# Kernel tuning notes

Measured on AMD Instinct MI355X. Metric: run time of the kernel, lower is better.

Reference implementation:

```python
import jax, jax.numpy as jnp
import numpy as np
from jax import lax

N = 100000   # input points
M = 100000   # output points
CIN = 64
COUT = 64
K = 3        # cubic kernel size
G = 50       # grid side (points live at voxel centers of a G^3 grid)
SHIFT = 1    # coordinate shift so border queries (coord -1) stay non-negative
B = 64       # per-axis encode base, > G + K; key fits easily in int32


def _encode(c):
    # c: [..., 3] int32 xyz voxel coords -> unique int32 key
    c = c + SHIFT
    return (c[..., 2] * B + c[..., 1]) * B + c[..., 0]


def setup_inputs() -> dict:
    rng = np.random.RandomState(0)
    total = G ** 3

    def decode(idx):
        x = idx % G
        y = (idx // G) % G
        z = idx // (G * G)
        # +0.5 moves points to voxel centers (as in the layer's docstring example)
        return np.stack([x, y, z], axis=1).astype(np.float32) + 0.5

    inp_positions = jnp.asarray(decode(rng.permutation(total)[:N]))
    out_positions = jnp.asarray(decode(rng.permutation(total)[:M]))

    key = jax.random.key(0)
    k1, k2 = jax.random.split(key, 2)
    inp_features = jax.random.normal(k1, (N, CIN), jnp.float32)
    kernel = jax.random.normal(k2, (K, K, K, CIN, COUT), jnp.float32) * 0.05
    bias = jnp.zeros((COUT,), jnp.float32)
    voxel_size = jnp.ones((), jnp.float32)
    return {
        "inp_features": inp_features,
        "inp_positions": inp_positions,
        "out_positions": out_positions,
        "voxel_size": voxel_size,
        "kernel": kernel,
        "bias": bias,
    }


def reference(inp_features, inp_positions, out_positions, voxel_size, kernel, bias):
    # SparseConv on a regular grid: odd cubic kernel -> offset = 0, Linf radius
    # K*voxel*0.51 selects exactly the K^3 voxel neighborhood. Nearest-neighbor
    # interpolation with identity mapping maps relative offset d in [-r, r]^3
    # to filter tap index d + r on each axis (x = width = last spatial dim).
    inp_coord = jnp.floor(inp_positions / voxel_size).astype(jnp.int32)  # [N,3]
    out_coord = jnp.floor(out_positions / voxel_size).astype(jnp.int32)  # [M,3]

    # sorted-key hash table over input voxels
    keys = _encode(inp_coord)                    # [N]
    order = jnp.argsort(keys)
    skeys = keys[order]
    feats = inp_features[order]                  # [N, Cin]

    r = K // 2
    K3 = K ** 3
    ks = jnp.arange(K3)
    # flat kernel order is (z, y, x) to match kernel.reshape(K3, Cin, Cout)
    d_xyz = jnp.stack([ks % K - r, (ks // K) % K - r, ks // (K * K) - r],
                      axis=1).astype(jnp.int32)  # [K3, 3]
    Kmat = kernel.reshape(K3, CIN, COUT)

    n_inp = skeys.shape[0]

    def step(acc, xs):
        d, W = xs                                 # d: [3], W: [Cin, Cout]
        qk = _encode(out_coord + d)               # [M]
        p = jnp.searchsorted(skeys, qk)
        pc = jnp.clip(p, 0, n_inp - 1)
        found = (skeys[pc] == qk)[:, None]        # [M, 1]
        g = jnp.where(found, feats[pc], 0.0)      # [M, Cin]
        return acc + g @ W, None

    out0 = jnp.zeros((out_coord.shape[0], COUT), inp_features.dtype)
    out, _ = lax.scan(step, out0, (d_xyz, Kmat))
    return out + bias
```

## Files before the change

kernel.cpp:

```cpp
#include <hip/hip_runtime.h>
#include <math.h>

#define GY 54
#define ZD 58
#define NROWS (ZD*GY*64)

#define HX 10
#define HY 6
#define HXY 60
#define NH 600
#define NBX 7
#define NBY 13
#define NBZ 7
#define NBRICK (NBX*NBY*NBZ)
#define SLAB 80

#define K3CC (27*64*64)

typedef __bf16  bf16x8 __attribute__((ext_vector_type(8)));
typedef float  f32x16 __attribute__((ext_vector_type(16)));

#define AS1 __attribute__((address_space(1)))
#define AS3 __attribute__((address_space(3)))
#define GLD_LDS16(g, l) \
    __builtin_amdgcn_global_load_lds((const AS1 void*)(g), (AS3 void*)(l), 16, 0, 0)

__global__ void prep_kernel(const float* __restrict__ ipos, int n,
                            const float* __restrict__ opos, int m,
                            const float* __restrict__ vsp,
                            const float* __restrict__ W,
                            const float* __restrict__ feats,
                            int* __restrict__ imap, int* __restrict__ ikey,
                            int* __restrict__ omap, int* __restrict__ okey,
                            __bf16* __restrict__ Wt4,
                            __bf16* __restrict__ zrow,
                            __bf16* __restrict__ featsB) {
    int i = blockIdx.x * 256 + threadIdx.x;
    float vs = vsp[0];
    if (i < n) {
        int x = (int)floorf(ipos[3*i+0] / vs) + 1;
        int y = (int)floorf(ipos[3*i+1] / vs) + 1;
        int z = (int)floorf(ipos[3*i+2] / vs) + 1;
        int key = (z * GY + y) * 64 + x;
        ikey[i] = key;
        imap[key] = i;
    } else if (i < n + m) {
        int j = i - n;
        int x = (int)floorf(opos[3*j+0] / vs) + 1;
        int y = (int)floorf(opos[3*j+1] / vs) + 1;
        int z = (int)floorf(opos[3*j+2] / vs) + 1;
        int key = (z * GY + y) * 64 + x;
        okey[j] = key;
        omap[key] = j;
    } else if (i < n + m + K3CC) {
        int k  = i - n - m;
        int t  = k >> 12;
        int r  = k & 4095;
        int ci = r >> 6;
        int co = r & 63;
        int p   = ci >> 4;
        int cil = ci & 15;
        Wt4[(((p * 27 + t) << 6) + co) * 16 + cil] = (__bf16)W[k];
    } else if (i < n + m + K3CC + 32) {
        zrow[i - n - m - K3CC] = (__bf16)0.f;
    } else {
        int j = i - n - m - K3CC - 32;
        if (j < n * 8) {
            const float4* s = (const float4*)(feats + (size_t)j * 8);
            float4 f0 = s[0], f1 = s[1];
            bf16x8 v;
            v[0]=(__bf16)f0.x; v[1]=(__bf16)f0.y; v[2]=(__bf16)f0.z; v[3]=(__bf16)f0.w;
            v[4]=(__bf16)f1.x; v[5]=(__bf16)f1.y; v[6]=(__bf16)f1.z; v[7]=(__bf16)f1.w;
            *(bf16x8*)(featsB + (size_t)j * 8) = v;
        }
    }
}

#define TAP_BODY(t)                                                            \
    {                                                                          \
        const int drow = ((t)/9 - 1)*HXY + (((t)/3)%3 - 1)*HX + ((t)%3 - 1);   \
        bf16x8 a0 = *(const bf16x8*)(Ab0 + drow * 16);                         \
        bf16x8 a1 = *(const bf16x8*)(Ab0 + (drow + HXY) * 16);                 \
        bf16x8 b0 = *(const bf16x8*)(Bg0 + (t) * 1024);                        \
        bf16x8 b1 = *(const bf16x8*)(Bg0 + (t) * 1024 + 512);                  \
        acc00 = __builtin_amdgcn_mfma_f32_32x32x16_bf16(a0, b0, acc00, 0, 0, 0); \
        acc01 = __builtin_amdgcn_mfma_f32_32x32x16_bf16(a0, b1, acc01, 0, 0, 0); \
        acc10 = __builtin_amdgcn_mfma_f32_32x32x16_bf16(a1, b0, acc10, 0, 0, 0); \
        acc11 = __builtin_amdgcn_mfma_f32_32x32x16_bf16(a1, b1, acc11, 0, 0, 0); \
    }

__global__ __launch_bounds__(256, 2) void conv_kernel(
    const __bf16* __restrict__ featsB,
    const __bf16* __restrict__ Wt4,
    const __bf16* __restrict__ zrow,
    const float* __restrict__ bias,
    const int*   __restrict__ imap,
    const int*   __restrict__ ikey,
    const int*   __restrict__ omap,
    const int*   __restrict__ okey,
    float*       __restrict__ out,
    int N, int M)
{
    __shared__ __align__(16) __bf16 halo[2 * NH * 16];
    __shared__ int ridx[NH];
    __shared__ int obuf[256];

    const int tid = threadIdx.x;

    int q = (blockIdx.x & 7) * SLAB + (blockIdx.x >> 3);
    if (q >= NBRICK) return;
    const int bx = q % NBX;
    int rem = q / NBX;
    const int by = rem % NBY;
    const int bz = rem / NBY;

    #pragma unroll
    for (int it = 0; it < 3; ++it) {
        int r = it * 256 + tid;
        if (r < NH) {
            int xs = r % HX;
            int t2 = r / HX;
            int ys = t2 % HY;
            int zs = t2 / HY;
            int key = ((bz*8 + zs) * GY + (by*4 + ys)) * 64 + (bx*8 + xs);
            int idx = imap[key];
            int c = min(max(idx, 0), N - 1);
            ridx[r] = (idx >= 0 && idx < N && ikey[c] == key) ? idx : -1;
        }
    }
    {
        int x = tid & 7, y = (tid >> 3) & 3, z = tid >> 5;
        int key = ((bz*8 + z + 1) * GY + (by*4 + y + 1)) * 64 + (bx*8 + x + 1);
        int o = omap[key];
        int c = min(max(o, 0), M - 1);
        obuf[tid] = (o >= 0 && o < M && okey[c] == key) ? o : -1;
    }

    const int wave  = tid >> 6;
    const int lane  = tid & 63;
    const int lrow  = lane & 31;
    const int halfk = lane >> 5;
    const int xv = lrow & 7, yv = (lrow >> 3) & 3;
    const int arow0 = (2*wave + 1) * HXY + (yv + 1) * HX + (xv + 1);

    f32x16 acc00, acc01, acc10, acc11;
    #pragma unroll
    for (int i = 0; i < 16; ++i) { acc00[i]=0.f; acc01[i]=0.f; acc10[i]=0.f; acc11[i]=0.f; }

    __syncthreads();

    #pragma unroll
    for (int it = 0; it < 5; ++it) {
        int task = it * 256 + tid;
        if (task < NH * 2) {
            int r  = task >> 1;
            int hl = task & 1;
            int idx = ridx[r];
            const __bf16* src = (idx >= 0) ? featsB + (size_t)idx * 64 + hl * 8
                                           : zrow;
            GLD_LDS16(src, (char*)halo + task * 16);
        }
    }
    __syncthreads();

    #pragma unroll 1
    for (int p = 0; p < 4; ++p) {
        if (p < 3) {
            char* dst = (char*)halo + ((p + 1) & 1) * (NH * 16 * 2);
            #pragma unroll
            for (int it = 0; it < 5; ++it) {
                int task = it * 256 + tid;
                if (task < NH * 2) {
                    int r  = task >> 1;
                    int hl = task & 1;
                    int idx = ridx[r];
                    const __bf16* src = (idx >= 0)
                        ? featsB + (size_t)idx * 64 + (p + 1) * 16 + hl * 8
                        : zrow;
                    GLD_LDS16(src, dst + task * 16);
                }
            }
        }

        const __bf16* Ab0 = halo + (p & 1) * (NH * 16) + arow0 * 16 + halfk * 8;
        const __bf16* Bg0 = Wt4 + (size_t)p * 27648 + lrow * 16 + halfk * 8;

        #pragma unroll
        for (int t = 0; t < 27; ++t) TAP_BODY(t)

        if (p < 3) __syncthreads();
    }

    const int col0 = lrow, col1 = 32 + lrow;
    const float bv0 = bias[col0], bv1 = bias[col1];
    #pragma unroll
    for (int r = 0; r < 16; ++r) {
        int mrow = (r & 3) + 8 * (r >> 2) + 4 * halfk;
        int o0 = obuf[(2*wave)     * 32 + mrow];
        int o1 = obuf[(2*wave + 1) * 32 + mrow];
        if (o0 >= 0) {
            out[(size_t)o0 * 64 + col0] = acc00[r] + bv0;
            out[(size_t)o0 * 64 + col1] = acc01[r] + bv1;
        }
        if (o1 >= 0) {
            out[(size_t)o1 * 64 + col0] = acc10[r] + bv0;
            out[(size_t)o1 * 64 + col1] = acc11[r] + bv1;
        }
    }
}

extern "C" void kernel_launch(void* const* d_in, const int* in_sizes, int n_in,
                              void* d_out, int out_size, void* d_ws, size_t ws_size,
                              hipStream_t stream) {
    const float* feats = (const float*)d_in[0];
    const float* ipos  = (const float*)d_in[1];
    const float* opos  = (const float*)d_in[2];
    const float* vsp   = (const float*)d_in[3];
    const float* W     = (const float*)d_in[4];
    const float* bias  = (const float*)d_in[5];

    int N = in_sizes[0] / 64;
    int M = out_size / 64;

    int*    imap   = (int*)d_ws;
    int*    omap   = imap + NROWS;
    int*    ikey   = omap + NROWS;
    int*    okey   = ikey + N;
    __bf16* Wt4    = (__bf16*)(okey + M);
    __bf16* zrow   = Wt4 + K3CC;
    __bf16* featsB = zrow + 32;

    int total = N + M + K3CC + 32 + N * 8;
    prep_kernel<<<(total + 255) / 256, 256, 0, stream>>>(ipos, N, opos, M, vsp, W, feats,
                                                         imap, ikey, omap, okey,
                                                         Wt4, zrow, featsB);
    conv_kernel<<<8 * SLAB, 256, 0, stream>>>(featsB, Wt4, zrow, bias,
                                              imap, ikey, omap, okey,
                                              (float*)d_out, N, M);
}
```

Baseline: 133.5 us.

## Split input-channel reduction across two blocks per brick with atomic accumulation

Each spatial brick is now handled by two blocks, each covering half of the input-channel chunks. Partial sums are combined with float atomicAdd into an output that the prep kernel pre-fills with bias. This doubles the grid and halves the per-block halo LDS footprint to raise occupancy and parallelism. In exchange, the halo gather and index lookup run twice per brick, the output is written atomically and needs an extra fill pass, the double-buffered prefetch is replaced by a synchronous reload, and the result order becomes nondeterministic.

```diff
diff --git a/kernel.cpp b/kernel.cpp
--- a/kernel.cpp
+++ b/kernel.cpp
@@ -13,7 +13,9 @@
 #define NBY 13
 #define NBZ 7
 #define NBRICK (NBX*NBY*NBZ)
-#define SLAB 80
+
+#define NBLK (2*NBRICK)
+#define SLAB2 160
 
 #define K3CC (27*64*64)
 
@@ -30,11 +32,13 @@
                             const float* __restrict__ vsp,
                             const float* __restrict__ W,
                             const float* __restrict__ feats,
+                            const float* __restrict__ bias,
                             int* __restrict__ imap, int* __restrict__ ikey,
                             int* __restrict__ omap, int* __restrict__ okey,
                             __bf16* __restrict__ Wt4,
                             __bf16* __restrict__ zrow,
-                            __bf16* __restrict__ featsB) {
+                            __bf16* __restrict__ featsB,
+                            float* __restrict__ out) {
     int i = blockIdx.x * 256 + threadIdx.x;
     float vs = vsp[0];
     if (i < n) {
@@ -72,6 +76,14 @@
             v[0]=(__bf16)f0.x; v[1]=(__bf16)f0.y; v[2]=(__bf16)f0.z; v[3]=(__bf16)f0.w;
             v[4]=(__bf16)f1.x; v[5]=(__bf16)f1.y; v[6]=(__bf16)f1.z; v[7]=(__bf16)f1.w;
             *(bf16x8*)(featsB + (size_t)j * 8) = v;
+        } else {
+            int j2 = j - n * 8;
+            if (j2 < m * 4) {
+                const float4* b4 = (const float4*)bias;
+                float4* o4 = (float4*)out + (size_t)j2 * 4;
+                int c4 = (j2 & 3) * 4;
+                o4[0] = b4[c4]; o4[1] = b4[c4+1]; o4[2] = b4[c4+2]; o4[3] = b4[c4+3];
+            }
         }
     }
 }
@@ -93,7 +105,6 @@
     const __bf16* __restrict__ featsB,
     const __bf16* __restrict__ Wt4,
     const __bf16* __restrict__ zrow,
-    const float* __restrict__ bias,
     const int*   __restrict__ imap,
     const int*   __restrict__ ikey,
     const int*   __restrict__ omap,
@@ -101,16 +112,18 @@
     float*       __restrict__ out,
     int N, int M)
 {
-    __shared__ __align__(16) __bf16 halo[2 * NH * 16];
+    __shared__ __align__(16) __bf16 halo[NH * 16];
     __shared__ int ridx[NH];
     __shared__ int obuf[256];
 
     const int tid = threadIdx.x;
 
-    int q = (blockIdx.x & 7) * SLAB + (blockIdx.x >> 3);
-    if (q >= NBRICK) return;
-    const int bx = q % NBX;
-    int rem = q / NBX;
+    int q = (blockIdx.x & 7) * SLAB2 + (blockIdx.x >> 3);
+    if (q >= NBLK) return;
+    const int brick = q >> 1;
+    const int s     = q & 1;
+    const int bx = brick % NBX;
+    int rem = brick / NBX;
     const int by = rem % NBY;
     const int bz = rem / NBY;
 
@@ -156,17 +169,19 @@
             int r  = task >> 1;
             int hl = task & 1;
             int idx = ridx[r];
-            const __bf16* src = (idx >= 0) ? featsB + (size_t)idx * 64 + hl * 8
-                                           : zrow;
+            const __bf16* src = (idx >= 0)
+                ? featsB + (size_t)idx * 64 + 2*s*16 + hl * 8
+                : zrow;
             GLD_LDS16(src, (char*)halo + task * 16);
         }
     }
     __syncthreads();
 
     #pragma unroll 1
-    for (int p = 0; p < 4; ++p) {
-        if (p < 3) {
-            char* dst = (char*)halo + ((p + 1) & 1) * (NH * 16 * 2);
+    for (int pi = 0; pi < 2; ++pi) {
+        const int p = 2*s + pi;
+        if (pi) {
+            __syncthreads();
             #pragma unroll
             for (int it = 0; it < 5; ++it) {
                 int task = it * 256 + tid;
@@ -175,36 +190,34 @@
                     int hl = task & 1;
                     int idx = ridx[r];
                     const __bf16* src = (idx >= 0)
-                        ? featsB + (size_t)idx * 64 + (p + 1) * 16 + hl * 8
+                        ? featsB + (size_t)idx * 64 + p * 16 + hl * 8
                         : zrow;
-                    GLD_LDS16(src, dst + task * 16);
+                    GLD_LDS16(src, (char*)halo + task * 16);
                 }
             }
-        }
-
-        const __bf16* Ab0 = halo + (p & 1) * (NH * 16) + arow0 * 16 + halfk * 8;
+            __syncthreads();
+        }
+
+        const __bf16* Ab0 = halo + arow0 * 16 + halfk * 8;
         const __bf16* Bg0 = Wt4 + (size_t)p * 27648 + lrow * 16 + halfk * 8;
 
         #pragma unroll
         for (int t = 0; t < 27; ++t) TAP_BODY(t)
-
-        if (p < 3) __syncthreads();
     }
 
     const int col0 = lrow, col1 = 32 + lrow;
-    const float bv0 = bias[col0], bv1 = bias[col1];
     #pragma unroll
     for (int r = 0; r < 16; ++r) {
         int mrow = (r & 3) + 8 * (r >> 2) + 4 * halfk;
         int o0 = obuf[(2*wave)     * 32 + mrow];
         int o1 = obuf[(2*wave + 1) * 32 + mrow];
         if (o0 >= 0) {
-            out[(size_t)o0 * 64 + col0] = acc00[r] + bv0;
-            out[(size_t)o0 * 64 + col1] = acc01[r] + bv1;
+            atomicAdd(out + (size_t)o0 * 64 + col0, acc00[r]);
+            atomicAdd(out + (size_t)o0 * 64 + col1, acc01[r]);
         }
         if (o1 >= 0) {
-            out[(size_t)o1 * 64 + col0] = acc10[r] + bv0;
-            out[(size_t)o1 * 64 + col1] = acc11[r] + bv1;
+            atomicAdd(out + (size_t)o1 * 64 + col0, acc10[r]);
+            atomicAdd(out + (size_t)o1 * 64 + col1, acc11[r]);
         }
     }
 }
@@ -230,11 +243,11 @@
     __bf16* zrow   = Wt4 + K3CC;
     __bf16* featsB = zrow + 32;
 
-    int total = N + M + K3CC + 32 + N * 8;
+    int total = N + M + K3CC + 32 + N * 8 + M * 4;
     prep_kernel<<<(total + 255) / 256, 256, 0, stream>>>(ipos, N, opos, M, vsp, W, feats,
-                                                         imap, ikey, omap, okey,
-                                                         Wt4, zrow, featsB);
-    conv_kernel<<<8 * SLAB, 256, 0, stream>>>(featsB, Wt4, zrow, bias,
-                                              imap, ikey, omap, okey,
-                                              (float*)d_out, N, M);
+                                                         bias, imap, ikey, omap, okey,
+                                                         Wt4, zrow, featsB, (float*)d_out);
+    conv_kernel<<<8 * SLAB2, 256, 0, stream>>>(featsB, Wt4, zrow,
+                                               imap, ikey, omap, okey,
+                                               (float*)d_out, N, M);
 }
```

Measured after the change: 168.5 us. +26.2%, slower.

## Load full 64-channel halo once and loop taps by z-plane

Applied to the files above, without the earlier changes.

Replaces the double-buffered, four-pass channel pipeline with a single load of all 64 input channels for the whole halo into LDS (about 77KB), followed by one sync and a dz/tap/channel-chunk loop of MFMAs. This removes three intermediate barriers and the per-pass gather issue. In exchange, the gather no longer overlaps with compute, and the larger LDS footprint may cut occupancy below two blocks per CU. LDS reads now use a 128-byte row stride, which may cause more bank conflicts.

```diff
diff --git a/kernel.cpp b/kernel.cpp
--- a/kernel.cpp
+++ b/kernel.cpp
@@ -76,19 +76,6 @@
     }
 }
 
-#define TAP_BODY(t)                                                            \
-    {                                                                          \
-        const int drow = ((t)/9 - 1)*HXY + (((t)/3)%3 - 1)*HX + ((t)%3 - 1);   \
-        bf16x8 a0 = *(const bf16x8*)(Ab0 + drow * 16);                         \
-        bf16x8 a1 = *(const bf16x8*)(Ab0 + (drow + HXY) * 16);                 \
-        bf16x8 b0 = *(const bf16x8*)(Bg0 + (t) * 1024);                        \
-        bf16x8 b1 = *(const bf16x8*)(Bg0 + (t) * 1024 + 512);                  \
-        acc00 = __builtin_amdgcn_mfma_f32_32x32x16_bf16(a0, b0, acc00, 0, 0, 0); \
-        acc01 = __builtin_amdgcn_mfma_f32_32x32x16_bf16(a0, b1, acc01, 0, 0, 0); \
-        acc10 = __builtin_amdgcn_mfma_f32_32x32x16_bf16(a1, b0, acc10, 0, 0, 0); \
-        acc11 = __builtin_amdgcn_mfma_f32_32x32x16_bf16(a1, b1, acc11, 0, 0, 0); \
-    }
-
 __global__ __launch_bounds__(256, 2) void conv_kernel(
     const __bf16* __restrict__ featsB,
     const __bf16* __restrict__ Wt4,
@@ -101,7 +88,7 @@
     float*       __restrict__ out,
     int N, int M)
 {
-    __shared__ __align__(16) __bf16 halo[2 * NH * 16];
+    __shared__ __align__(16) __bf16 halo[NH * 64];
     __shared__ int ridx[NH];
     __shared__ int obuf[256];
 
@@ -150,45 +137,41 @@
     __syncthreads();
 
     #pragma unroll
-    for (int it = 0; it < 5; ++it) {
+    for (int it = 0; it < 19; ++it) {
         int task = it * 256 + tid;
-        if (task < NH * 2) {
-            int r  = task >> 1;
-            int hl = task & 1;
+        if (task < NH * 8) {
+            int r = task >> 3;
+            int c = task & 7;
             int idx = ridx[r];
-            const __bf16* src = (idx >= 0) ? featsB + (size_t)idx * 64 + hl * 8
+            const __bf16* src = (idx >= 0) ? featsB + (size_t)idx * 64 + c * 8
                                            : zrow;
             GLD_LDS16(src, (char*)halo + task * 16);
         }
     }
     __syncthreads();
 
+    const __bf16* Ab  = halo + arow0 * 64 + halfk * 8;
+    const __bf16* Bg0 = Wt4 + lrow * 16 + halfk * 8;
+
     #pragma unroll 1
-    for (int p = 0; p < 4; ++p) {
-        if (p < 3) {
-            char* dst = (char*)halo + ((p + 1) & 1) * (NH * 16 * 2);
+    for (int dz = 0; dz < 3; ++dz) {
+        const __bf16* Az = Ab + (dz - 1) * (HXY * 64);
+        const __bf16* Bz = Bg0 + dz * 9 * 1024;
+        #pragma unroll
+        for (int tq = 0; tq < 9; ++tq) {
+            const int drow = (tq / 3 - 1) * HX + (tq % 3 - 1);
             #pragma unroll
-            for (int it = 0; it < 5; ++it) {
-                int task = it * 256 + tid;
-                if (task < NH * 2) {
-                    int r  = task >> 1;
-                    int hl = task & 1;
-                    int idx = ridx[r];
-                    const __bf16* src = (idx >= 0)
-                        ? featsB + (size_t)idx * 64 + (p + 1) * 16 + hl * 8
-                        : zrow;
-                    GLD_LDS16(src, dst + task * 16);
-                }
+            for (int p = 0; p < 4; ++p) {
+                bf16x8 a0 = *(const bf16x8*)(Az + drow * 64 + p * 16);
+                bf16x8 a1 = *(const bf16x8*)(Az + (drow + HXY) * 64 + p * 16);
+                bf16x8 b0 = *(const bf16x8*)(Bz + tq * 1024 + p * 27648);
+                bf16x8 b1 = *(const bf16x8*)(Bz + tq * 1024 + p * 27648 + 512);
+                acc00 = __builtin_amdgcn_mfma_f32_32x32x16_bf16(a0, b0, acc00, 0, 0, 0);
+                acc01 = __builtin_amdgcn_mfma_f32_32x32x16_bf16(a0, b1, acc01, 0, 0, 0);
+                acc10 = __builtin_amdgcn_mfma_f32_32x32x16_bf16(a1, b0, acc10, 0, 0, 0);
+                acc11 = __builtin_amdgcn_mfma_f32_32x32x16_bf16(a1, b1, acc11, 0, 0, 0);
             }
         }
-
-        const __bf16* Ab0 = halo + (p & 1) * (NH * 16) + arow0 * 16 + halfk * 8;
-        const __bf16* Bg0 = Wt4 + (size_t)p * 27648 + lrow * 16 + halfk * 8;
-
-        #pragma unroll
-        for (int t = 0; t < 27; ++t) TAP_BODY(t)
-
-        if (p < 3) __syncthreads();
     }
 
     const int col0 = lrow, col1 = 32 + lrow;
```

Measured after the change: 161.2 us. 1.21x slower.
